# Kernel optimization log

Hardware: AMD Instinct MI355X
Metric: run time of the kernel (lower is better)

Reference implementation:

```python
import jax, jax.numpy as jnp
import numpy as np

B, N, C, K = 4, 1024, 384, 10


def _sqdist(a, b):
    # a: [B,P,3], b: [B,M,3] -> [B,P,M] squared euclidean distance
    d = (jnp.sum(a * a, -1)[:, :, None] + jnp.sum(b * b, -1)[:, None, :]
         - 2.0 * jnp.einsum('bpc,bmc->bpm', a, b))
    return jnp.maximum(d, 0.0)


def _gather(points, idx):
    # points: [B,M,C], idx: [B,...] int -> [B,...,C]  (index_points)
    return jax.vmap(lambda p, i: p[i])(points, idx)


def setup_inputs() -> dict:
    key = jax.random.key(0)
    ks = jax.random.split(key, 8)
    def lin(k_, fan_in, fan_out):
        return jax.random.normal(k_, (fan_in, fan_out), jnp.float32) * (1.0 / np.sqrt(fan_in))
    return {
        'q': jax.random.normal(ks[0], (B, N, C), jnp.float32),
        'q_pos': jax.random.normal(ks[1], (B, N, 3), jnp.float32),
        'Wv': lin(ks[2], C, C), 'bv': jnp.zeros((C,), jnp.float32),
        'W1': lin(ks[3], 2 * C, C), 'b1': jnp.zeros((C,), jnp.float32),
        'ln_g': jnp.ones((C,), jnp.float32), 'ln_b': jnp.zeros((C,), jnp.float32),
        'W2': lin(ks[4], C, 3),
        'Wk': lin(ks[5], 2 * C, C), 'bk': jnp.zeros((C,), jnp.float32),
    }


def reference(q, q_pos, Wv, bv, W1, b1, ln_g, ln_b, W2, Wk, bk):
    Bq, Nq, Cq = q.shape
    # 1) KNN of each query among all points (self-attn: v=q, v_pos=q_pos)
    d = _sqdist(q_pos, q_pos)                      # [B,N,N]
    _, idx = jax.lax.top_k(-d, K)                  # [B,N,K] (smallest distances)
    # 2) offset prediction from gathered projected features + query feature
    v_off = q @ Wv + bv                            # [B,N,C]
    off_local_v = _gather(v_off, idx)              # [B,N,K,C]
    qk = jnp.broadcast_to(q[:, :, None, :], (Bq, Nq, K, Cq))
    shift_feat = jnp.concatenate([off_local_v, qk], -1)  # [B,N,K,2C]
    h = shift_feat @ W1 + b1
    mu = jnp.mean(h, -1, keepdims=True)
    var = jnp.var(h, -1, keepdims=True)
    h = (h - mu) / jnp.sqrt(var + 1e-5) * ln_g + ln_b     # LayerNorm
    h = jax.nn.gelu(h, approximate=False)
    offset = jnp.tanh(h @ W2)                      # [B,N,K,3]
    # 3) deformed positions, scaled by half the local bbox extent
    local_v_pos = _gather(q_pos, idx)              # [B,N,K,3]
    scale = (local_v_pos.max(-2) - local_v_pos.min(-2))[:, :, None, :] * 0.5
    shift_pos = (local_v_pos + offset * scale).reshape(Bq, Nq * K, 3)
    # 4) three_nn + three_interpolate (inverse-squared-distance weights)
    d2 = _sqdist(shift_pos, q_pos)                 # [B,NK,N]
    negd, idx3 = jax.lax.top_k(-d2, 3)             # [B,NK,3]
    dist = -negd
    w = 1.0 / (dist + 1e-8)
    w = w / jnp.sum(w, -1, keepdims=True)
    feats3 = _gather(q, idx3)                      # [B,NK,3,C]
    interp = jnp.einsum('bpt,bptc->bpc', w, feats3).reshape(Bq, Nq, K, Cq)
    # 5) graph conv: concat(diff, q) -> Linear -> LeakyReLU(0.2) -> max over K
    feature = jnp.concatenate([interp - qk, qk], -1)      # [B,N,K,2C]
    out = jax.nn.leaky_relu(feature @ Wk + bk, negative_slope=0.2)
    return out.max(-2)                             # [B,N,C]
```

## Files before the change

### kernel.cpp

```cpp
#include <hip/hip_runtime.h>
#include <math.h>

#define BB 4
#define NN 1024
#define CC 384
#define KK 10
#define NKK (NN*KK)

typedef __attribute__((ext_vector_type(8))) short short8v;
typedef __attribute__((ext_vector_type(8))) unsigned short ushort8v;
typedef __attribute__((ext_vector_type(4))) float f32x4;

template <int NA>
__device__ __forceinline__ void wave_sum_arr(float* a) {
  #pragma unroll
  for (int off = 32; off > 0; off >>= 1) {
    float t[NA];
    #pragma unroll
    for (int u = 0; u < NA; ++u) t[u] = __shfl_xor(a[u], off, 64);
    #pragma unroll
    for (int u = 0; u < NA; ++u) a[u] += t[u];
  }
}

__device__ __forceinline__ unsigned short f2bf(float x) {
  unsigned int b = __float_as_uint(x);
  return (unsigned short)((b + 0x7fffu + ((b >> 16) & 1u)) >> 16);
}
__device__ __forceinline__ float bf2f(unsigned short h) {
  return __uint_as_float(((unsigned int)h) << 16);
}

#define NB_CVT  (BB * NN * CC / 1024)
#define NB_PB   (2 * CC * CC / 256)
#define NB_PREP (NB_CVT + NB_PB + 3)
__global__ __launch_bounds__(256) void prep_gemm_kernel(
    const float* __restrict__ q,
    const float* __restrict__ W1, const float* __restrict__ b1,
    const float* __restrict__ bv, const float* __restrict__ bk,
    const float* __restrict__ Wk, const float* __restrict__ Wv,
    unsigned short* __restrict__ qh, unsigned short* __restrict__ ql,
    unsigned short* __restrict__ Wt,
    float* __restrict__ bias_uv, float* __restrict__ bias_pb,
    float* __restrict__ M1p) {
  int blk = blockIdx.x;
  int tid = threadIdx.x;
  if (blk < NB_CVT) {
    int i = (blk * 256 + tid) * 4;
    float4 v = *reinterpret_cast<const float4*>(q + i);
    float x[4] = {v.x, v.y, v.z, v.w};
    #pragma unroll
    for (int j = 0; j < 4; ++j) {
      unsigned short h = f2bf(x[j]);
      qh[i + j] = h;
      ql[i + j] = f2bf(x[j] - bf2f(h));
    }
    return;
  }
  if (blk < NB_CVT + NB_PB) {
    int idx = (blk - NB_CVT) * 256 + tid;
    int n = idx / CC, k = idx % CC;
    float v;
    if (n < CC) v = Wk[(size_t)k * CC + n];
    else        v = Wk[(size_t)CC * CC + k * CC + (n - CC)] - Wk[(size_t)k * CC + (n - CC)];
    Wt[(size_t)n * CC + k] = f2bf(v);
    return;
  }
  if (blk < NB_PREP) {
    int j = (blk - NB_CVT - NB_PB) * 256 + tid;
    if (j >= 2 * CC) return;
    if (j < CC) { bias_uv[j] = 0.f; bias_pb[j] = 0.f; }
    else {
      int c = j - CC;
      float s = b1[c];
      for (int i = 0; i < CC; ++i) s += bv[i] * W1[i * CC + c];
      bias_uv[j] = s;
      bias_pb[j] = bk[c];
    }
    return;
  }
  {
    int r = blk - NB_PREP;
    int bx = r % 3, by = (r / 3) % 3, bz = r / 9;
    __shared__ float As[16][132];
    __shared__ float Bs[16][128];
    int tx = tid & 15, ty = tid >> 4;
    int row0 = by * 128, col0 = bx * 128;
    int k0 = bz * 48;
    float acc[8][8] = {};
    int arow = tid >> 2, akc = (tid & 3) << 2;
    int brow = tid >> 5, bcol = (tid & 31) << 2;
    for (int kt = k0; kt < k0 + 48; kt += 16) {
      #pragma unroll
      for (int h = 0; h < 2; ++h) {
        int rr = arow + 64 * h;
        float4 av = *reinterpret_cast<const float4*>(Wv + (size_t)(row0 + rr) * CC + kt + akc);
        As[akc + 0][rr] = av.x; As[akc + 1][rr] = av.y;
        As[akc + 2][rr] = av.z; As[akc + 3][rr] = av.w;
      }
      #pragma unroll
      for (int h = 0; h < 2; ++h) {
        int rr = brow + 8 * h;
        float4 bv4 = *reinterpret_cast<const float4*>(W1 + (size_t)(kt + rr) * CC + col0 + bcol);
        *reinterpret_cast<float4*>(&Bs[rr][bcol]) = bv4;
      }
      __syncthreads();
      #pragma unroll
      for (int kk = 0; kk < 16; ++kk) {
        float4 a0 = *reinterpret_cast<const float4*>(&As[kk][ty << 2]);
        float4 a1 = *reinterpret_cast<const float4*>(&As[kk][64 + (ty << 2)]);
        float4 b0 = *reinterpret_cast<const float4*>(&Bs[kk][tx << 2]);
        float4 b1 = *reinterpret_cast<const float4*>(&Bs[kk][64 + (tx << 2)]);
        float av_[8] = {a0.x, a0.y, a0.z, a0.w, a1.x, a1.y, a1.z, a1.w};
        float bv_[8] = {b0.x, b0.y, b0.z, b0.w, b1.x, b1.y, b1.z, b1.w};
        #pragma unroll
        for (int i = 0; i < 8; ++i)
          #pragma unroll
          for (int j = 0; j < 8; ++j) acc[i][j] += av_[i] * bv_[j];
      }
      __syncthreads();
    }
    float* Cz = M1p + (size_t)bz * CC * CC;
    #pragma unroll
    for (int i = 0; i < 8; ++i) {
      int row = row0 + (ty << 2) + (i & 3) + ((i & 4) << 4);
      if (row >= CC) continue;
      #pragma unroll
      for (int h = 0; h < 2; ++h) {
        int col = col0 + 64 * h + (tx << 2);
        if (col >= CC) continue;
        float4 rv;
        rv.x = acc[i][4 * h + 0]; rv.y = acc[i][4 * h + 1];
        rv.z = acc[i][4 * h + 2]; rv.w = acc[i][4 * h + 3];
        *reinterpret_cast<float4*>(Cz + (size_t)row * CC + col) = rv;
      }
    }
  }
}

__global__ void pack_uv_split_kernel(const float* __restrict__ M1p, const float* __restrict__ W1,
                                     unsigned short* __restrict__ Buvh,
                                     unsigned short* __restrict__ Buvl) {
  int idx = blockIdx.x * 256 + threadIdx.x;
  int k = idx / (2 * CC), n = idx % (2 * CC);
  float val;
  if (n < CC) {
    float s = 0.f;
    #pragma unroll
    for (int p = 0; p < 8; ++p) s += M1p[(size_t)p * CC * CC + (size_t)k * CC + n];
    val = s;
  } else {
    val = W1[(size_t)(CC + k) * CC + (n - CC)];
  }
  unsigned short h = f2bf(val);
  Buvh[(size_t)n * CC + k] = h;
  Buvl[(size_t)n * CC + k] = f2bf(val - bf2f(h));
}

__global__ __launch_bounds__(256) void gemm_mfma_kernel(
    const unsigned short* __restrict__ qh, const unsigned short* __restrict__ ql,
    const unsigned short* __restrict__ Buvh, const unsigned short* __restrict__ Buvl,
    const unsigned short* __restrict__ Wt,
    float* __restrict__ Cuv, float* __restrict__ Cpb,
    const float* __restrict__ bias_uv, const float* __restrict__ bias_pb) {
  int path = blockIdx.z;
  const unsigned short* Bh = path ? Wt : Buvh;
  float* Cm = path ? Cpb : Cuv;
  const float* bias = path ? bias_pb : bias_uv;
  __shared__ unsigned short Ah[128 * 32], Alo[128 * 32];
  __shared__ unsigned short Bhs[128 * 32], Bls[128 * 32];
  int tid = threadIdx.x;
  int lane = tid & 63, w = tid >> 6;
  int m0 = blockIdx.y * 128, n0 = blockIdx.x * 128;
  f32x4 acc[4][4];
  #pragma unroll
  for (int i = 0; i < 4; ++i)
    #pragma unroll
    for (int j = 0; j < 4; ++j) acc[i][j] = (f32x4){0.f, 0.f, 0.f, 0.f};
  int rl = lane & 15, kg = lane >> 4;
  for (int k0 = 0; k0 < CC; k0 += 32) {
    #pragma unroll
    for (int j = 0; j < 2; ++j) {
      int id = tid + 256 * j;
      int r = id >> 2, s = id & 3;
      int sw = (s ^ (r & 3)) * 8;
      *reinterpret_cast<ushort8v*>(Ah + r * 32 + sw) =
          *reinterpret_cast<const ushort8v*>(qh + (size_t)(m0 + r) * CC + k0 + s * 8);
      *reinterpret_cast<ushort8v*>(Bhs + r * 32 + sw) =
          *reinterpret_cast<const ushort8v*>(Bh + (size_t)(n0 + r) * CC + k0 + s * 8);
      if (!path) {
        *reinterpret_cast<ushort8v*>(Alo + r * 32 + sw) =
            *reinterpret_cast<const ushort8v*>(ql + (size_t)(m0 + r) * CC + k0 + s * 8);
        *reinterpret_cast<ushort8v*>(Bls + r * 32 + sw) =
            *reinterpret_cast<const ushort8v*>(Buvl + (size_t)(n0 + r) * CC + k0 + s * 8);
      }
    }
    __syncthreads();
    short8v afh[4], bfh[4], afl[4], bfl[4];
    #pragma unroll
    for (int f = 0; f < 4; ++f) {
      int ar = (w & 1) * 64 + f * 16 + rl;
      int aof = ar * 32 + (kg ^ (ar & 3)) * 8;
      int br = (w >> 1) * 64 + f * 16 + rl;
      int bof = br * 32 + (kg ^ (br & 3)) * 8;
      afh[f] = *reinterpret_cast<const short8v*>(Ah + aof);
      bfh[f] = *reinterpret_cast<const short8v*>(Bhs + bof);
      if (!path) {
        afl[f] = *reinterpret_cast<const short8v*>(Alo + aof);
        bfl[f] = *reinterpret_cast<const short8v*>(Bls + bof);
      }
    }
    #pragma unroll
    for (int i = 0; i < 4; ++i) {
      #pragma unroll
      for (int j = 0; j < 4; ++j) {
        acc[i][j] = __builtin_amdgcn_mfma_f32_16x16x32_bf16(afh[i], bfh[j], acc[i][j], 0, 0, 0);
        if (!path) {
          acc[i][j] = __builtin_amdgcn_mfma_f32_16x16x32_bf16(afh[i], bfl[j], acc[i][j], 0, 0, 0);
          acc[i][j] = __builtin_amdgcn_mfma_f32_16x16x32_bf16(afl[i], bfh[j], acc[i][j], 0, 0, 0);
        }
      }
    }
    __syncthreads();
  }
  #pragma unroll
  for (int i = 0; i < 4; ++i) {
    #pragma unroll
    for (int j = 0; j < 4; ++j) {
      int col = n0 + (w >> 1) * 64 + j * 16 + rl;
      float bcol_v = bias[col];
      #pragma unroll
      for (int r = 0; r < 4; ++r) {
        int row = m0 + (w & 1) * 64 + i * 16 + kg * 4 + r;
        Cm[(size_t)row * (2 * CC) + col] = acc[i][j][r] + bcol_v;
      }
    }
  }
}

__global__ __launch_bounds__(256) void knn_kernel(
    const float* __restrict__ q_pos, int* __restrict__ idxk, float* __restrict__ meta) {
  int blk = blockIdx.x;
  int b = blk >> 8;
  int ng = blk & 255;
  int tid = threadIdx.x;
  int wave = tid >> 6, lane = tid & 63;
  int n = ng * 4 + wave;
  int bn = b * NN + n;
  __shared__ float4 sp4[NN];

  const float* qp = q_pos + (size_t)b * NN * 3;
  for (int i = tid; i < NN; i += 256) {
    float x = qp[i * 3 + 0], y = qp[i * 3 + 1], z = qp[i * 3 + 2];
    sp4[i] = (float4){x, y, z, x * x + y * y + z * z};
  }
  __syncthreads();

  int nb[KK];
  {
    float4 me = sp4[n];
    float px = me.x, py = me.y, pz = me.z, sp = me.w;
    float bd[KK]; int bi[KK];
    #pragma unroll
    for (int s = 0; s < KK; ++s) { bd[s] = 1e30f; bi[s] = -1; }
    #pragma unroll 4
    for (int j = 0; j < 16; ++j) {
      int m = lane + (j << 6);
      float4 c = sp4[m];
      float dot = fmaf(px, c.x, fmaf(py, c.y, pz * c.z));
      float d = fmaf(-2.f, dot, sp + c.w);
      d = fmaxf(d, 0.f);
      if (d < bd[KK - 1]) {
        bd[KK - 1] = d; bi[KK - 1] = m;
        #pragma unroll
        for (int s = KK - 1; s >= 1; --s) {
          if (bd[s] < bd[s - 1]) {
            float td = bd[s]; bd[s] = bd[s - 1]; bd[s - 1] = td;
            int ti = bi[s]; bi[s] = bi[s - 1]; bi[s - 1] = ti;
          }
        }
      }
    }
    #pragma unroll
    for (int s = 0; s < KK; ++s) {
      float d = bd[0]; int i = bi[0];
      #pragma unroll
      for (int off = 32; off > 0; off >>= 1) {
        float od = __shfl_xor(d, off, 64);
        int oi = __shfl_xor(i, off, 64);
        if (od < d || (od == d && oi < i)) { d = od; i = oi; }
      }
      if (bi[0] == i) {
        #pragma unroll
        for (int u = 0; u < KK - 1; ++u) { bd[u] = bd[u + 1]; bi[u] = bi[u + 1]; }
        bd[KK - 1] = 1e30f; bi[KK - 1] = -1;
      }
      nb[s] = i;
    }
  }

  float sclx, scly, sclz;
  {
    float mxx = -1e30f, mnx = 1e30f, mxy = -1e30f, mny = 1e30f, mxz = -1e30f, mnz = 1e30f;
    #pragma unroll
    for (int k2 = 0; k2 < KK; ++k2) {
      float4 c = sp4[nb[k2]];
      mxx = fmaxf(mxx, c.x); mnx = fminf(mnx, c.x);
      mxy = fmaxf(mxy, c.y); mny = fminf(mny, c.y);
      mxz = fmaxf(mxz, c.z); mnz = fminf(mnz, c.z);
    }
    sclx = (mxx - mnx) * 0.5f; scly = (mxy - mny) * 0.5f; sclz = (mxz - mnz) * 0.5f;
  }

  int myn = 0;
  #pragma unroll
  for (int k = 0; k < KK; ++k) if (lane == k) myn = nb[k];
  float* mrow = meta + (size_t)bn * 36;
  if (lane < KK) {
    idxk[(size_t)bn * KK + lane] = myn;
    float4 c = sp4[myn];
    mrow[lane * 3 + 0] = c.x;
    mrow[lane * 3 + 1] = c.y;
    mrow[lane * 3 + 2] = c.z;
  }
  if (lane == 0) { mrow[30] = sclx; mrow[31] = scly; mrow[32] = sclz; }
}

__global__ __launch_bounds__(256) void mlp_kernel(
    const float* __restrict__ Cat_uv, const float* __restrict__ lng, const float* __restrict__ lnb,
    const float* __restrict__ W2, const int* __restrict__ idxk, const float* __restrict__ meta,
    float* __restrict__ shp) {
  int tid = threadIdx.x;
  int wave = tid >> 6, lane = tid & 63;
  int bn = blockIdx.x * 2 + (wave >> 1);
  int b = bn >> 10;
  int kb = (wave & 1) * 5;

  int nb5[5];
  #pragma unroll
  for (int kk = 0; kk < 5; ++kk) nb5[kk] = idxk[(size_t)bn * KK + kb + kk];

  float Vv[6], lg[6], lb[6], w2a[6], w2b[6], w2c[6];
  const float* Vrow = Cat_uv + (size_t)bn * (2 * CC) + CC;
  #pragma unroll
  for (int i = 0; i < 6; ++i) {
    int c = lane + (i << 6);
    Vv[i] = Vrow[c];
    lg[i] = lng[c]; lb[i] = lnb[c];
    w2a[i] = W2[c * 3 + 0]; w2b[i] = W2[c * 3 + 1]; w2c[i] = W2[c * 3 + 2];
  }

  float hk[5][6];
  float sum[5];
  #pragma unroll
  for (int kk = 0; kk < 5; ++kk) {
    const float* Urow = Cat_uv + ((size_t)b * NN + nb5[kk]) * (2 * CC);
    float s = 0.f;
    #pragma unroll
    for (int i = 0; i < 6; ++i) {
      hk[kk][i] = Urow[lane + (i << 6)] + Vv[i];
      s += hk[kk][i];
    }
    sum[kk] = s;
  }
  wave_sum_arr<5>(sum);
  float mu[5], var[5];
  #pragma unroll
  for (int kk = 0; kk < 5; ++kk) {
    mu[kk] = sum[kk] * (1.0f / CC);
    float v = 0.f;
    #pragma unroll
    for (int i = 0; i < 6; ++i) { float d = hk[kk][i] - mu[kk]; v += d * d; }
    var[kk] = v;
  }
  wave_sum_arr<5>(var);
  float o[15];
  #pragma unroll
  for (int kk = 0; kk < 5; ++kk) {
    float rstd = 1.0f / sqrtf(var[kk] * (1.0f / CC) + 1e-5f);
    float o0 = 0.f, o1 = 0.f, o2 = 0.f;
    #pragma unroll
    for (int i = 0; i < 6; ++i) {
      float x = (hk[kk][i] - mu[kk]) * rstd * lg[i] + lb[i];
      float g = 0.5f * x * (1.0f + erff(x * 0.70710678118654752440f));
      o0 = fmaf(g, w2a[i], o0); o1 = fmaf(g, w2b[i], o1); o2 = fmaf(g, w2c[i], o2);
    }
    o[kk * 3 + 0] = o0; o[kk * 3 + 1] = o1; o[kk * 3 + 2] = o2;
  }
  wave_sum_arr<15>(o);
  float ox = 0.f, oy = 0.f, oz = 0.f;
  #pragma unroll
  for (int kk = 0; kk < 5; ++kk) {
    if (lane == kb + kk) { ox = o[kk * 3 + 0]; oy = o[kk * 3 + 1]; oz = o[kk * 3 + 2]; }
  }
  if (lane >= kb && lane < kb + 5) {
    const float* mrow = meta + (size_t)bn * 36;
    float lvx = mrow[lane * 3 + 0], lvy = mrow[lane * 3 + 1], lvz = mrow[lane * 3 + 2];
    float sclx = mrow[30], scly = mrow[31], sclz = mrow[32];
    float* sp = shp + ((size_t)bn * KK + lane) * 3;
    sp[0] = lvx + tanhf(ox) * sclx;
    sp[1] = lvy + tanhf(oy) * scly;
    sp[2] = lvz + tanhf(oz) * sclz;
  }
}

__global__ __launch_bounds__(256) void interp_kernel(
    const float* __restrict__ Cat_pb, const float* __restrict__ q_pos,
    const float* __restrict__ shp, float* __restrict__ out) {
  int bn = blockIdx.x;
  int b = bn >> 10;
  int tid = threadIdx.x;
  int wave = tid >> 6, lane = tid & 63;
  __shared__ float4 sp4[NN];
  __shared__ float s_shp[KK * 3];
  __shared__ float s_w[KK][3];
  __shared__ int s_i[KK][3];

  const float* qp = q_pos + (size_t)b * NN * 3;
  for (int i = tid; i < NN; i += 256) {
    float x = qp[i * 3 + 0], y = qp[i * 3 + 1], z = qp[i * 3 + 2];
    sp4[i] = (float4){x, y, z, x * x + y * y + z * z};
  }
  if (tid < KK * 3) s_shp[tid] = shp[(size_t)bn * KK * 3 + tid];
  __syncthreads();

  int cnt = (wave < 2) ? 3 : 2;
  int pbase = (wave < 2) ? wave * 3 : 6 + (wave - 2) * 2;
  float px[3], py[3], pz[3], ps[3];
  #pragma unroll
  for (int j = 0; j < 3; ++j) {
    int p = pbase + (j < cnt ? j : cnt - 1);
    px[j] = s_shp[p * 3 + 0]; py[j] = s_shp[p * 3 + 1]; pz[j] = s_shp[p * 3 + 2];
    ps[j] = fmaf(px[j], px[j], fmaf(py[j], py[j], pz[j] * pz[j]));
  }
  float d0[3], d1[3], d2[3]; int i0[3], i1[3], i2[3];
  #pragma unroll
  for (int j = 0; j < 3; ++j) { d0[j] = d1[j] = d2[j] = 1e30f; i0[j] = i1[j] = i2[j] = -1; }
  #pragma unroll 4
  for (int it = 0; it < 16; ++it) {
    int m = lane + (it << 6);
    float4 c = sp4[m];
    #pragma unroll
    for (int j = 0; j < 3; ++j) {
      float dot = fmaf(px[j], c.x, fmaf(py[j], c.y, pz[j] * c.z));
      float d = fmaf(-2.f, dot, ps[j] + c.w);
      d = fmaxf(d, 0.f);
      bool c2 = d < d2[j], c1 = d < d1[j], c0 = d < d0[j];
      d2[j] = c1 ? d1[j] : (c2 ? d : d2[j]);  i2[j] = c1 ? i1[j] : (c2 ? m : i2[j]);
      d1[j] = c0 ? d0[j] : (c1 ? d : d1[j]);  i1[j] = c0 ? i0[j] : (c1 ? m : i1[j]);
      d0[j] = c0 ? d : d0[j];                 i0[j] = c0 ? m : i0[j];
    }
  }
  float wd[3][3]; int wi[3][3];
  #pragma unroll
  for (int s = 0; s < 3; ++s) {
    float d[3]; int ii[3];
    #pragma unroll
    for (int j = 0; j < 3; ++j) { d[j] = d0[j]; ii[j] = i0[j]; }
    #pragma unroll
    for (int off = 32; off > 0; off >>= 1) {
      #pragma unroll
      for (int j = 0; j < 3; ++j) {
        float od = __shfl_xor(d[j], off, 64);
        int oi = __shfl_xor(ii[j], off, 64);
        if (od < d[j] || (od == d[j] && oi < ii[j])) { d[j] = od; ii[j] = oi; }
      }
    }
    #pragma unroll
    for (int j = 0; j < 3; ++j) {
      if (i0[j] == ii[j]) {
        d0[j] = d1[j]; i0[j] = i1[j]; d1[j] = d2[j]; i1[j] = i2[j]; d2[j] = 1e30f; i2[j] = -1;
      }
      wd[s][j] = d[j]; wi[s][j] = ii[j];
    }
  }
  if (lane == 0) {
    #pragma unroll
    for (int j = 0; j < 3; ++j) {
      if (j < cnt) {
        float w0 = 1.f / (wd[0][j] + 1e-8f), w1 = 1.f / (wd[1][j] + 1e-8f), w2 = 1.f / (wd[2][j] + 1e-8f);
        float s = w0 + w1 + w2;
        int p = pbase + j;
        s_w[p][0] = w0 / s; s_w[p][1] = w1 / s; s_w[p][2] = w2 / s;
        s_i[p][0] = wi[0][j]; s_i[p][1] = wi[1][j]; s_i[p][2] = wi[2][j];
      }
    }
  }
  __syncthreads();

  const float* Pb = Cat_pb + (size_t)b * NN * (2 * CC);
  const float* BseRow = Cat_pb + (size_t)bn * (2 * CC) + CC;
  for (int c = tid; c < CC; c += 256) {
    float base = BseRow[c];
    float best = -1e30f;
    #pragma unroll
    for (int k = 0; k < KK; ++k) {
      float acc = base;
      #pragma unroll
      for (int tt = 0; tt < 3; ++tt)
        acc = fmaf(s_w[k][tt], Pb[(size_t)s_i[k][tt] * (2 * CC) + c], acc);
      acc = acc >= 0.f ? acc : 0.2f * acc;
      best = fmaxf(best, acc);
    }
    out[(size_t)bn * CC + c] = best;
  }
}

extern "C" void kernel_launch(void* const* d_in, const int* in_sizes, int n_in,
                              void* d_out, int out_size, void* d_ws, size_t ws_size,
                              hipStream_t stream) {
  (void)in_sizes; (void)n_in; (void)out_size; (void)ws_size;
  const float* q    = (const float*)d_in[0];
  const float* qpos = (const float*)d_in[1];
  const float* Wv   = (const float*)d_in[2];
  const float* bv   = (const float*)d_in[3];
  const float* W1   = (const float*)d_in[4];
  const float* b1   = (const float*)d_in[5];
  const float* lng  = (const float*)d_in[6];
  const float* lnb  = (const float*)d_in[7];
  const float* W2   = (const float*)d_in[8];
  const float* Wk   = (const float*)d_in[9];
  const float* bk   = (const float*)d_in[10];
  float* out = (float*)d_out;

  float* ws = (float*)d_ws;
  float* Cat_uv = ws; ws += (size_t)BB * NN * 2 * CC;
  float* Cat_pb = ws; ws += (size_t)BB * NN * 2 * CC;
  float* M1p = Cat_pb;
  float* bias_uv = ws; ws += 2 * CC;
  float* bias_pb = ws; ws += 2 * CC;
  float* shp = ws; ws += (size_t)BB * NKK * 3;
  float* meta = ws; ws += (size_t)BB * NN * 36;
  unsigned short* qh = (unsigned short*)ws;  ws += (size_t)BB * NN * CC / 2;
  unsigned short* ql = (unsigned short*)ws;  ws += (size_t)BB * NN * CC / 2;
  unsigned short* Wt = (unsigned short*)ws;  ws += (size_t)2 * CC * CC / 2;
  unsigned short* Buvh = (unsigned short*)ws; ws += (size_t)2 * CC * CC / 2;
  unsigned short* Buvl = (unsigned short*)ws; ws += (size_t)2 * CC * CC / 2;
  int* idxk = (int*)ws;

  prep_gemm_kernel<<<dim3(NB_PREP + 72), dim3(256), 0, stream>>>(
      q, W1, b1, bv, bk, Wk, Wv, qh, ql, Wt, bias_uv, bias_pb, M1p);
  pack_uv_split_kernel<<<dim3(CC * 2 * CC / 256), dim3(256), 0, stream>>>(M1p, W1, Buvh, Buvl);
  gemm_mfma_kernel<<<dim3(2 * CC / 128, BB * NN / 128, 2), dim3(256), 0, stream>>>(
      qh, ql, Buvh, Buvl, Wt, Cat_uv, Cat_pb, bias_uv, bias_pb);
  knn_kernel<<<dim3(BB * NN / 4), dim3(256), 0, stream>>>(qpos, idxk, meta);
  mlp_kernel<<<dim3(BB * NN / 2), dim3(256), 0, stream>>>(
      Cat_uv, lng, lnb, W2, idxk, meta, shp);
  interp_kernel<<<dim3(BB * NN), dim3(256), 0, stream>>>(
      Cat_pb, qpos, shp, out);
}
```

Measured before the change: 148.6 us.

## Split KNN and three-NN candidate scans across two waves with shared-memory merge

The KNN kernel now gives each query two waves, each scanning half of the 1024 candidates. The two partial top-10 lists are merged in shared memory with a rank-based selection. The interp kernel likewise splits the candidate range across wave pairs, each handling 5 shifted points, and merges the partial top-3 lists in shared memory. This halves the serial scan length per wave but adds block syncs, a merge step, and twice as many KNN blocks, each reloading the point cloud into LDS.

Measured after the change: 166.6 us. 12.1% more time.

```diff
diff --git a/kernel.cpp b/kernel.cpp
--- a/kernel.cpp
+++ b/kernel.cpp
@@ -241,13 +241,17 @@
 __global__ __launch_bounds__(256) void knn_kernel(
     const float* __restrict__ q_pos, int* __restrict__ idxk, float* __restrict__ meta) {
   int blk = blockIdx.x;
-  int b = blk >> 8;
-  int ng = blk & 255;
+  int b = blk >> 9;
+  int ng = blk & 511;
   int tid = threadIdx.x;
   int wave = tid >> 6, lane = tid & 63;
-  int n = ng * 4 + wave;
+  int qi = wave >> 1, ch = wave & 1;
+  int n = ng * 2 + qi;
   int bn = b * NN + n;
   __shared__ float4 sp4[NN];
+  __shared__ float s_hd[2][2][KK];
+  __shared__ int   s_hi[2][2][KK];
+  __shared__ int   s_nb[2][KK];
 
   const float* qp = q_pos + (size_t)b * NN * 3;
   for (int i = tid; i < NN; i += 256) {
@@ -256,7 +260,6 @@
   }
   __syncthreads();
 
-  int nb[KK];
   {
     float4 me = sp4[n];
     float px = me.x, py = me.y, pz = me.z, sp = me.w;
@@ -264,8 +267,8 @@
     #pragma unroll
     for (int s = 0; s < KK; ++s) { bd[s] = 1e30f; bi[s] = -1; }
     #pragma unroll 4
-    for (int j = 0; j < 16; ++j) {
-      int m = lane + (j << 6);
+    for (int j = 0; j < 8; ++j) {
+      int m = (ch << 9) + lane + (j << 6);
       float4 c = sp4[m];
       float dot = fmaf(px, c.x, fmaf(py, c.y, pz * c.z));
       float d = fmaf(-2.f, dot, sp + c.w);
@@ -281,6 +284,7 @@
         }
       }
     }
+    float myd = 0.f; int myi = -1;
     #pragma unroll
     for (int s = 0; s < KK; ++s) {
       float d = bd[0]; int i = bi[0];
@@ -295,9 +299,30 @@
         for (int u = 0; u < KK - 1; ++u) { bd[u] = bd[u + 1]; bi[u] = bi[u + 1]; }
         bd[KK - 1] = 1e30f; bi[KK - 1] = -1;
       }
-      nb[s] = i;
-    }
-  }
+      if (lane == s) { myd = d; myi = i; }
+    }
+    if (lane < KK) { s_hd[qi][ch][lane] = myd; s_hi[qi][ch][lane] = myi; }
+  }
+  __syncthreads();
+  if (ch == 1) return;
+
+  {
+    const float* hd = &s_hd[qi][0][0];
+    const int*   hi = &s_hi[qi][0][0];
+    int sl = (lane < 20) ? lane : 0;
+    float md = hd[sl];
+    int   mi = hi[sl];
+    int rank = 0;
+    #pragma unroll
+    for (int j = 0; j < 20; ++j) {
+      float dj = hd[j]; int ij = hi[j];
+      rank += ((dj < md) || (dj == md && ij < mi)) ? 1 : 0;
+    }
+    if (lane < 20 && rank < KK) s_nb[qi][rank] = mi;
+  }
+  int nb[KK];
+  #pragma unroll
+  for (int s = 0; s < KK; ++s) nb[s] = s_nb[qi][s];
 
   float sclx, scly, sclz;
   {
@@ -411,8 +436,11 @@
   int b = bn >> 10;
   int tid = threadIdx.x;
   int wave = tid >> 6, lane = tid & 63;
+  int pg = wave >> 1, ch = wave & 1;
   __shared__ float4 sp4[NN];
   __shared__ float s_shp[KK * 3];
+  __shared__ float s_pd[2][2][5][3];
+  __shared__ int   s_pi[2][2][5][3];
   __shared__ float s_w[KK][3];
   __shared__ int s_i[KK][3];
 
@@ -424,24 +452,22 @@
   if (tid < KK * 3) s_shp[tid] = shp[(size_t)bn * KK * 3 + tid];
   __syncthreads();
 
-  int cnt = (wave < 2) ? 3 : 2;
-  int pbase = (wave < 2) ? wave * 3 : 6 + (wave - 2) * 2;
-  float px[3], py[3], pz[3], ps[3];
-  #pragma unroll
-  for (int j = 0; j < 3; ++j) {
-    int p = pbase + (j < cnt ? j : cnt - 1);
+  float px[5], py[5], pz[5], ps[5];
+  #pragma unroll
+  for (int j = 0; j < 5; ++j) {
+    int p = pg * 5 + j;
     px[j] = s_shp[p * 3 + 0]; py[j] = s_shp[p * 3 + 1]; pz[j] = s_shp[p * 3 + 2];
     ps[j] = fmaf(px[j], px[j], fmaf(py[j], py[j], pz[j] * pz[j]));
   }
-  float d0[3], d1[3], d2[3]; int i0[3], i1[3], i2[3];
-  #pragma unroll
-  for (int j = 0; j < 3; ++j) { d0[j] = d1[j] = d2[j] = 1e30f; i0[j] = i1[j] = i2[j] = -1; }
-  #pragma unroll 4
-  for (int it = 0; it < 16; ++it) {
-    int m = lane + (it << 6);
+  float d0[5], d1[5], d2[5]; int i0[5], i1[5], i2[5];
+  #pragma unroll
+  for (int j = 0; j < 5; ++j) { d0[j] = d1[j] = d2[j] = 1e30f; i0[j] = i1[j] = i2[j] = -1; }
+  #pragma unroll 2
+  for (int it = 0; it < 8; ++it) {
+    int m = (ch << 9) + lane + (it << 6);
     float4 c = sp4[m];
     #pragma unroll
-    for (int j = 0; j < 3; ++j) {
+    for (int j = 0; j < 5; ++j) {
       float dot = fmaf(px[j], c.x, fmaf(py[j], c.y, pz[j] * c.z));
       float d = fmaf(-2.f, dot, ps[j] + c.w);
       d = fmaxf(d, 0.f);
@@ -451,40 +477,67 @@
       d0[j] = c0 ? d : d0[j];                 i0[j] = c0 ? m : i0[j];
     }
   }
-  float wd[3][3]; int wi[3][3];
+  float wd[3][5]; int wi[3][5];
   #pragma unroll
   for (int s = 0; s < 3; ++s) {
-    float d[3]; int ii[3];
-    #pragma unroll
-    for (int j = 0; j < 3; ++j) { d[j] = d0[j]; ii[j] = i0[j]; }
+    float d[5]; int ii[5];
+    #pragma unroll
+    for (int j = 0; j < 5; ++j) { d[j] = d0[j]; ii[j] = i0[j]; }
     #pragma unroll
     for (int off = 32; off > 0; off >>= 1) {
       #pragma unroll
-      for (int j = 0; j < 3; ++j) {
+      for (int j = 0; j < 5; ++j) {
         float od = __shfl_xor(d[j], off, 64);
         int oi = __shfl_xor(ii[j], off, 64);
         if (od < d[j] || (od == d[j] && oi < ii[j])) { d[j] = od; ii[j] = oi; }
       }
     }
     #pragma unroll
-    for (int j = 0; j < 3; ++j) {
+    for (int j = 0; j < 5; ++j) {
       if (i0[j] == ii[j]) {
         d0[j] = d1[j]; i0[j] = i1[j]; d1[j] = d2[j]; i1[j] = i2[j]; d2[j] = 1e30f; i2[j] = -1;
       }
       wd[s][j] = d[j]; wi[s][j] = ii[j];
     }
   }
-  if (lane == 0) {
-    #pragma unroll
-    for (int j = 0; j < 3; ++j) {
-      if (j < cnt) {
-        float w0 = 1.f / (wd[0][j] + 1e-8f), w1 = 1.f / (wd[1][j] + 1e-8f), w2 = 1.f / (wd[2][j] + 1e-8f);
-        float s = w0 + w1 + w2;
-        int p = pbase + j;
-        s_w[p][0] = w0 / s; s_w[p][1] = w1 / s; s_w[p][2] = w2 / s;
-        s_i[p][0] = wi[0][j]; s_i[p][1] = wi[1][j]; s_i[p][2] = wi[2][j];
-      }
-    }
+  {
+    float a0 = 0.f, a1 = 0.f, a2 = 0.f; int e0 = -1, e1 = -1, e2 = -1;
+    #pragma unroll
+    for (int j = 0; j < 5; ++j)
+      if (lane == j) { a0 = wd[0][j]; a1 = wd[1][j]; a2 = wd[2][j];
+                       e0 = wi[0][j]; e1 = wi[1][j]; e2 = wi[2][j]; }
+    if (lane < 5) {
+      s_pd[pg][ch][lane][0] = a0; s_pd[pg][ch][lane][1] = a1; s_pd[pg][ch][lane][2] = a2;
+      s_pi[pg][ch][lane][0] = e0; s_pi[pg][ch][lane][1] = e1; s_pi[pg][ch][lane][2] = e2;
+    }
+  }
+  __syncthreads();
+
+  if (wave == 0 && lane < KK) {
+    int g = lane / 5, j2 = lane % 5;
+    float ah = s_pd[g][0][j2][0], an1 = s_pd[g][0][j2][1], an2 = s_pd[g][0][j2][2];
+    int  aih = s_pi[g][0][j2][0], ain1 = s_pi[g][0][j2][1], ain2 = s_pi[g][0][j2][2];
+    float bh = s_pd[g][1][j2][0], bn1 = s_pd[g][1][j2][1], bn2 = s_pd[g][1][j2][2];
+    int  bih = s_pi[g][1][j2][0], bin1 = s_pi[g][1][j2][1], bin2 = s_pi[g][1][j2][2];
+    float o0, o1, o2; int q0, q1, q2;
+    #pragma unroll
+    for (int t = 0; t < 3; ++t) {
+      bool ta = ah <= bh;
+      float ov = ta ? ah : bh; int oq = ta ? aih : bih;
+      float nah = ta ? an1 : ah;  int naih = ta ? ain1 : aih;
+      float nan1 = ta ? an2 : an1; int nain1 = ta ? ain2 : ain1;
+      float nbh = ta ? bh : bn1;  int nbih = ta ? bih : bin1;
+      float nbn1 = ta ? bn1 : bn2; int nbin1 = ta ? bin1 : bin2;
+      ah = nah; an1 = nan1; aih = naih; ain1 = nain1;
+      bh = nbh; bn1 = nbn1; bih = nbih; bin1 = nbin1;
+      if (t == 0) { o0 = ov; q0 = oq; }
+      else if (t == 1) { o1 = ov; q1 = oq; }
+      else { o2 = ov; q2 = oq; }
+    }
+    float w0 = 1.f / (o0 + 1e-8f), w1 = 1.f / (o1 + 1e-8f), w2 = 1.f / (o2 + 1e-8f);
+    float s = w0 + w1 + w2;
+    s_w[lane][0] = w0 / s; s_w[lane][1] = w1 / s; s_w[lane][2] = w2 / s;
+    s_i[lane][0] = q0; s_i[lane][1] = q1; s_i[lane][2] = q2;
   }
   __syncthreads();
 
@@ -543,7 +596,7 @@
   pack_uv_split_kernel<<<dim3(CC * 2 * CC / 256), dim3(256), 0, stream>>>(M1p, W1, Buvh, Buvl);
   gemm_mfma_kernel<<<dim3(2 * CC / 128, BB * NN / 128, 2), dim3(256), 0, stream>>>(
       qh, ql, Buvh, Buvl, Wt, Cat_uv, Cat_pb, bias_uv, bias_pb);
-  knn_kernel<<<dim3(BB * NN / 4), dim3(256), 0, stream>>>(qpos, idxk, meta);
+  knn_kernel<<<dim3(BB * NN / 2), dim3(256), 0, stream>>>(qpos, idxk, meta);
   mlp_kernel<<<dim3(BB * NN / 2), dim3(256), 0, stream>>>(
       Cat_uv, lng, lnb, W2, idxk, meta, shp);
   interp_kernel<<<dim3(BB * NN), dim3(256), 0, stream>>>(
```

## Merge GEMM and KNN into one launch with block-index dispatch

Applied to the files above, without the earlier changes.

Combines the MFMA GEMM kernel and the independent KNN kernel into a single grid. The first 384 blocks run GEMM tiles and the remaining 1024 blocks run KNN, with both paths sharing one 32KB shared buffer. This removes one kernel launch and its serialization gap, and lets KNN blocks fill compute units the GEMM leaves idle. The cost is a larger shared-memory footprint for KNN blocks (32KB instead of 16KB), which may lower their occupancy, and register pressure now set by the heavier GEMM path.

Result: faster. 140.7 us (median of 2 runs) (-5.3%).

```diff
diff --git a/kernel.cpp b/kernel.cpp
--- a/kernel.cpp
+++ b/kernel.cpp
@@ -157,173 +157,182 @@
   Buvl[(size_t)n * CC + k] = f2bf(val - bf2f(h));
 }
 
-__global__ __launch_bounds__(256) void gemm_mfma_kernel(
+#define GEMM_NB 384
+__global__ __launch_bounds__(256) void gemm_knn_kernel(
     const unsigned short* __restrict__ qh, const unsigned short* __restrict__ ql,
     const unsigned short* __restrict__ Buvh, const unsigned short* __restrict__ Buvl,
     const unsigned short* __restrict__ Wt,
     float* __restrict__ Cuv, float* __restrict__ Cpb,
-    const float* __restrict__ bias_uv, const float* __restrict__ bias_pb) {
-  int path = blockIdx.z;
-  const unsigned short* Bh = path ? Wt : Buvh;
-  float* Cm = path ? Cpb : Cuv;
-  const float* bias = path ? bias_pb : bias_uv;
-  __shared__ unsigned short Ah[128 * 32], Alo[128 * 32];
-  __shared__ unsigned short Bhs[128 * 32], Bls[128 * 32];
+    const float* __restrict__ bias_uv, const float* __restrict__ bias_pb,
+    const float* __restrict__ q_pos, int* __restrict__ idxk, float* __restrict__ meta) {
+  __shared__ __align__(16) char smem[32768];
+  int blk = blockIdx.x;
   int tid = threadIdx.x;
-  int lane = tid & 63, w = tid >> 6;
-  int m0 = blockIdx.y * 128, n0 = blockIdx.x * 128;
-  f32x4 acc[4][4];
-  #pragma unroll
-  for (int i = 0; i < 4; ++i)
-    #pragma unroll
-    for (int j = 0; j < 4; ++j) acc[i][j] = (f32x4){0.f, 0.f, 0.f, 0.f};
-  int rl = lane & 15, kg = lane >> 4;
-  for (int k0 = 0; k0 < CC; k0 += 32) {
-    #pragma unroll
-    for (int j = 0; j < 2; ++j) {
-      int id = tid + 256 * j;
-      int r = id >> 2, s = id & 3;
-      int sw = (s ^ (r & 3)) * 8;
-      *reinterpret_cast<ushort8v*>(Ah + r * 32 + sw) =
-          *reinterpret_cast<const ushort8v*>(qh + (size_t)(m0 + r) * CC + k0 + s * 8);
-      *reinterpret_cast<ushort8v*>(Bhs + r * 32 + sw) =
-          *reinterpret_cast<const ushort8v*>(Bh + (size_t)(n0 + r) * CC + k0 + s * 8);
-      if (!path) {
-        *reinterpret_cast<ushort8v*>(Alo + r * 32 + sw) =
-            *reinterpret_cast<const ushort8v*>(ql + (size_t)(m0 + r) * CC + k0 + s * 8);
-        *reinterpret_cast<ushort8v*>(Bls + r * 32 + sw) =
-            *reinterpret_cast<const ushort8v*>(Buvl + (size_t)(n0 + r) * CC + k0 + s * 8);
-      }
+  int lane = tid & 63, wave = tid >> 6;
+
+  if (blk < GEMM_NB) {
+    int path = blk / 192;
+    int rem = blk % 192;
+    int by = rem / 6, bx = rem % 6;
+    unsigned short* Ah  = (unsigned short*)smem;
+    unsigned short* Alo = (unsigned short*)(smem + 8192);
+    unsigned short* Bhs = (unsigned short*)(smem + 16384);
+    unsigned short* Bls = (unsigned short*)(smem + 24576);
+    const unsigned short* Bh = path ? Wt : Buvh;
+    float* Cm = path ? Cpb : Cuv;
+    const float* bias = path ? bias_pb : bias_uv;
+    int m0 = by * 128, n0 = bx * 128;
+    f32x4 acc[4][4];
+    #pragma unroll
+    for (int i = 0; i < 4; ++i)
+      #pragma unroll
+      for (int j = 0; j < 4; ++j) acc[i][j] = (f32x4){0.f, 0.f, 0.f, 0.f};
+    int rl = lane & 15, kg = lane >> 4;
+    for (int k0 = 0; k0 < CC; k0 += 32) {
+      #pragma unroll
+      for (int j = 0; j < 2; ++j) {
+        int id = tid + 256 * j;
+        int r = id >> 2, s = id & 3;
+        int sw = (s ^ (r & 3)) * 8;
+        *reinterpret_cast<ushort8v*>(Ah + r * 32 + sw) =
+            *reinterpret_cast<const ushort8v*>(qh + (size_t)(m0 + r) * CC + k0 + s * 8);
+        *reinterpret_cast<ushort8v*>(Bhs + r * 32 + sw) =
+            *reinterpret_cast<const ushort8v*>(Bh + (size_t)(n0 + r) * CC + k0 + s * 8);
+        if (!path) {
+          *reinterpret_cast<ushort8v*>(Alo + r * 32 + sw) =
+              *reinterpret_cast<const ushort8v*>(ql + (size_t)(m0 + r) * CC + k0 + s * 8);
+          *reinterpret_cast<ushort8v*>(Bls + r * 32 + sw) =
+              *reinterpret_cast<const ushort8v*>(Buvl + (size_t)(n0 + r) * CC + k0 + s * 8);
+        }
+      }
+      __syncthreads();
+      short8v afh[4], bfh[4], afl[4], bfl[4];
+      #pragma unroll
+      for (int f = 0; f < 4; ++f) {
+        int ar = (wave & 1) * 64 + f * 16 + rl;
+        int aof = ar * 32 + (kg ^ (ar & 3)) * 8;
+        int br = (wave >> 1) * 64 + f * 16 + rl;
+        int bof = br * 32 + (kg ^ (br & 3)) * 8;
+        afh[f] = *reinterpret_cast<const short8v*>(Ah + aof);
+        bfh[f] = *reinterpret_cast<const short8v*>(Bhs + bof);
+        if (!path) {
+          afl[f] = *reinterpret_cast<const short8v*>(Alo + aof);
+          bfl[f] = *reinterpret_cast<const short8v*>(Bls + bof);
+        }
+      }
+      #pragma unroll
+      for (int i = 0; i < 4; ++i) {
+        #pragma unroll
+        for (int j = 0; j < 4; ++j) {
+          acc[i][j] = __builtin_amdgcn_mfma_f32_16x16x32_bf16(afh[i], bfh[j], acc[i][j], 0, 0, 0);
+          if (!path) {
+            acc[i][j] = __builtin_amdgcn_mfma_f32_16x16x32_bf16(afh[i], bfl[j], acc[i][j], 0, 0, 0);
+            acc[i][j] = __builtin_amdgcn_mfma_f32_16x16x32_bf16(afl[i], bfh[j], acc[i][j], 0, 0, 0);
+          }
+        }
+      }
+      __syncthreads();
+    }
+    #pragma unroll
+    for (int i = 0; i < 4; ++i) {
+      #pragma unroll
+      for (int j = 0; j < 4; ++j) {
+        int col = n0 + (wave >> 1) * 64 + j * 16 + rl;
+        float bcol_v = bias[col];
+        #pragma unroll
+        for (int r = 0; r < 4; ++r) {
+          int row = m0 + (wave & 1) * 64 + i * 16 + kg * 4 + r;
+          Cm[(size_t)row * (2 * CC) + col] = acc[i][j][r] + bcol_v;
+        }
+      }
+    }
+    return;
+  }
+
+  {
+    int kblk = blk - GEMM_NB;
+    int b = kblk >> 8;
+    int ng = kblk & 255;
+    int n = ng * 4 + wave;
+    int bn = b * NN + n;
+    float4* sp4 = (float4*)smem;
+
+    const float* qp = q_pos + (size_t)b * NN * 3;
+    for (int i = tid; i < NN; i += 256) {
+      float x = qp[i * 3 + 0], y = qp[i * 3 + 1], z = qp[i * 3 + 2];
+      sp4[i] = (float4){x, y, z, x * x + y * y + z * z};
     }
     __syncthreads();
-    short8v afh[4], bfh[4], afl[4], bfl[4];
-    #pragma unroll
-    for (int f = 0; f < 4; ++f) {
-      int ar = (w & 1) * 64 + f * 16 + rl;
-      int aof = ar * 32 + (kg ^ (ar & 3)) * 8;
-      int br = (w >> 1) * 64 + f * 16 + rl;
-      int bof = br * 32 + (kg ^ (br & 3)) * 8;
-      afh[f] = *reinterpret_cast<const short8v*>(Ah + aof);
-      bfh[f] = *reinterpret_cast<const short8v*>(Bhs + bof);
-      if (!path) {
-        afl[f] = *reinterpret_cast<const short8v*>(Alo + aof);
-        bfl[f] = *reinterpret_cast<const short8v*>(Bls + bof);
-      }
-    }
-    #pragma unroll
-    for (int i = 0; i < 4; ++i) {
-      #pragma unroll
-      for (int j = 0; j < 4; ++j) {
-        acc[i][j] = __builtin_amdgcn_mfma_f32_16x16x32_bf16(afh[i], bfh[j], acc[i][j], 0, 0, 0);
-        if (!path) {
-          acc[i][j] = __builtin_amdgcn_mfma_f32_16x16x32_bf16(afh[i], bfl[j], acc[i][j], 0, 0, 0);
-          acc[i][j] = __builtin_amdgcn_mfma_f32_16x16x32_bf16(afl[i], bfh[j], acc[i][j], 0, 0, 0);
-        }
-      }
-    }
-    __syncthreads();
-  }
-  #pragma unroll
-  for (int i = 0; i < 4; ++i) {
-    #pragma unroll
-    for (int j = 0; j < 4; ++j) {
-      int col = n0 + (w >> 1) * 64 + j * 16 + rl;
-      float bcol_v = bias[col];
-      #pragma unroll
-      for (int r = 0; r < 4; ++r) {
-        int row = m0 + (w & 1) * 64 + i * 16 + kg * 4 + r;
-        Cm[(size_t)row * (2 * CC) + col] = acc[i][j][r] + bcol_v;
-      }
-    }
-  }
-}
-
-__global__ __launch_bounds__(256) void knn_kernel(
-    const float* __restrict__ q_pos, int* __restrict__ idxk, float* __restrict__ meta) {
-  int blk = blockIdx.x;
-  int b = blk >> 8;
-  int ng = blk & 255;
-  int tid = threadIdx.x;
-  int wave = tid >> 6, lane = tid & 63;
-  int n = ng * 4 + wave;
-  int bn = b * NN + n;
-  __shared__ float4 sp4[NN];
-
-  const float* qp = q_pos + (size_t)b * NN * 3;
-  for (int i = tid; i < NN; i += 256) {
-    float x = qp[i * 3 + 0], y = qp[i * 3 + 1], z = qp[i * 3 + 2];
-    sp4[i] = (float4){x, y, z, x * x + y * y + z * z};
-  }
-  __syncthreads();
-
-  int nb[KK];
-  {
-    float4 me = sp4[n];
-    float px = me.x, py = me.y, pz = me.z, sp = me.w;
-    float bd[KK]; int bi[KK];
-    #pragma unroll
-    for (int s = 0; s < KK; ++s) { bd[s] = 1e30f; bi[s] = -1; }
-    #pragma unroll 4
-    for (int j = 0; j < 16; ++j) {
-      int m = lane + (j << 6);
-      float4 c = sp4[m];
-      float dot = fmaf(px, c.x, fmaf(py, c.y, pz * c.z));
-      float d = fmaf(-2.f, dot, sp + c.w);
-      d = fmaxf(d, 0.f);
-      if (d < bd[KK - 1]) {
-        bd[KK - 1] = d; bi[KK - 1] = m;
+
+    int nb[KK];
+    {
+      float4 me = sp4[n];
+      float px = me.x, py = me.y, pz = me.z, sp = me.w;
+      float bd[KK]; int bi[KK];
+      #pragma unroll
+      for (int s = 0; s < KK; ++s) { bd[s] = 1e30f; bi[s] = -1; }
+      #pragma unroll 4
+      for (int j = 0; j < 16; ++j) {
+        int m = lane + (j << 6);
+        float4 c = sp4[m];
+        float dot = fmaf(px, c.x, fmaf(py, c.y, pz * c.z));
+        float d = fmaf(-2.f, dot, sp + c.w);
+        d = fmaxf(d, 0.f);
+        if (d < bd[KK - 1]) {
+          bd[KK - 1] = d; bi[KK - 1] = m;
+          #pragma unroll
+          for (int s = KK - 1; s >= 1; --s) {
+            if (bd[s] < bd[s - 1]) {
+              float td = bd[s]; bd[s] = bd[s - 1]; bd[s - 1] = td;
+              int ti = bi[s]; bi[s] = bi[s - 1]; bi[s - 1] = ti;
+            }
+          }
+        }
+      }
+      #pragma unroll
+      for (int s = 0; s < KK; ++s) {
+        float d = bd[0]; int i = bi[0];
         #pragma unroll
-        for (int s = KK - 1; s >= 1; --s) {
-          if (bd[s] < bd[s - 1]) {
-            float td = bd[s]; bd[s] = bd[s - 1]; bd[s - 1] = td;
-            int ti = bi[s]; bi[s] = bi[s - 1]; bi[s - 1] = ti;
-          }
-        }
-      }
-    }
-    #pragma unroll
-    for (int s = 0; s < KK; ++s) {
-      float d = bd[0]; int i = bi[0];
-      #pragma unroll
-      for (int off = 32; off > 0; off >>= 1) {
-        float od = __shfl_xor(d, off, 64);
-        int oi = __shfl_xor(i, off, 64);
-        if (od < d || (od == d && oi < i)) { d = od; i = oi; }
-      }
-      if (bi[0] == i) {
-        #pragma unroll
-        for (int u = 0; u < KK - 1; ++u) { bd[u] = bd[u + 1]; bi[u] = bi[u + 1]; }
-        bd[KK - 1] = 1e30f; bi[KK - 1] = -1;
-      }
-      nb[s] = i;
-    }
-  }
-
-  float sclx, scly, sclz;
-  {
-    float mxx = -1e30f, mnx = 1e30f, mxy = -1e30f, mny = 1e30f, mxz = -1e30f, mnz = 1e30f;
-    #pragma unroll
-    for (int k2 = 0; k2 < KK; ++k2) {
-      float4 c = sp4[nb[k2]];
-      mxx = fmaxf(mxx, c.x); mnx = fminf(mnx, c.x);
-      mxy = fmaxf(mxy, c.y); mny = fminf(mny, c.y);
-      mxz = fmaxf(mxz, c.z); mnz = fminf(mnz, c.z);
-    }
-    sclx = (mxx - mnx) * 0.5f; scly = (mxy - mny) * 0.5f; sclz = (mxz - mnz) * 0.5f;
-  }
-
-  int myn = 0;
-  #pragma unroll
-  for (int k = 0; k < KK; ++k) if (lane == k) myn = nb[k];
-  float* mrow = meta + (size_t)bn * 36;
-  if (lane < KK) {
-    idxk[(size_t)bn * KK + lane] = myn;
-    float4 c = sp4[myn];
-    mrow[lane * 3 + 0] = c.x;
-    mrow[lane * 3 + 1] = c.y;
-    mrow[lane * 3 + 2] = c.z;
-  }
-  if (lane == 0) { mrow[30] = sclx; mrow[31] = scly; mrow[32] = sclz; }
+        for (int off = 32; off > 0; off >>= 1) {
+          float od = __shfl_xor(d, off, 64);
+          int oi = __shfl_xor(i, off, 64);
+          if (od < d || (od == d && oi < i)) { d = od; i = oi; }
+        }
+        if (bi[0] == i) {
+          #pragma unroll
+          for (int u = 0; u < KK - 1; ++u) { bd[u] = bd[u + 1]; bi[u] = bi[u + 1]; }
+          bd[KK - 1] = 1e30f; bi[KK - 1] = -1;
+        }
+        nb[s] = i;
+      }
+    }
+
+    float sclx, scly, sclz;
+    {
+      float mxx = -1e30f, mnx = 1e30f, mxy = -1e30f, mny = 1e30f, mxz = -1e30f, mnz = 1e30f;
+      #pragma unroll
+      for (int k2 = 0; k2 < KK; ++k2) {
+        float4 c = sp4[nb[k2]];
+        mxx = fmaxf(mxx, c.x); mnx = fminf(mnx, c.x);
+        mxy = fmaxf(mxy, c.y); mny = fminf(mny, c.y);
+        mxz = fmaxf(mxz, c.z); mnz = fminf(mnz, c.z);
+      }
+      sclx = (mxx - mnx) * 0.5f; scly = (mxy - mny) * 0.5f; sclz = (mxz - mnz) * 0.5f;
+    }
+
+    int myn = 0;
+    #pragma unroll
+    for (int k = 0; k < KK; ++k) if (lane == k) myn = nb[k];
+    float* mrow = meta + (size_t)bn * 36;
+    if (lane < KK) {
+      idxk[(size_t)bn * KK + lane] = myn;
+      float4 c = sp4[myn];
+      mrow[lane * 3 + 0] = c.x;
+      mrow[lane * 3 + 1] = c.y;
+      mrow[lane * 3 + 2] = c.z;
+    }
+    if (lane == 0) { mrow[30] = sclx; mrow[31] = scly; mrow[32] = sclz; }
+  }
 }
 
 __global__ __launch_bounds__(256) void mlp_kernel(
@@ -541,9 +550,8 @@
   prep_gemm_kernel<<<dim3(NB_PREP + 72), dim3(256), 0, stream>>>(
       q, W1, b1, bv, bk, Wk, Wv, qh, ql, Wt, bias_uv, bias_pb, M1p);
   pack_uv_split_kernel<<<dim3(CC * 2 * CC / 256), dim3(256), 0, stream>>>(M1p, W1, Buvh, Buvl);
-  gemm_mfma_kernel<<<dim3(2 * CC / 128, BB * NN / 128, 2), dim3(256), 0, stream>>>(
-      qh, ql, Buvh, Buvl, Wt, Cat_uv, Cat_pb, bias_uv, bias_pb);
-  knn_kernel<<<dim3(BB * NN / 4), dim3(256), 0, stream>>>(qpos, idxk, meta);
+  gemm_knn_kernel<<<dim3(GEMM_NB + BB * NN / 4), dim3(256), 0, stream>>>(
+      qh, ql, Buvh, Buvl, Wt, Cat_uv, Cat_pb, bias_uv, bias_pb, qpos, idxk, meta);
   mlp_kernel<<<dim3(BB * NN / 2), dim3(256), 0, stream>>>(
       Cat_uv, lng, lnb, W2, idxk, meta, shp);
   interp_kernel<<<dim3(BB * NN), dim3(256), 0, stream>>>(
```
